# Optimization experiments

Hardware: AMD Instinct MI355X
Metric: run time of the kernel (lower is better)

Reference implementation:

```python
import jax, jax.numpy as jnp
import numpy as np

SHAPES = [(96, 96), (48, 48), (24, 24), (12, 12)]
B, C, NH, NP, NL, LYR, DFF = 4, 256, 8, 3, 4, 3, 1024
HD = C // NH
N = sum(h * w for h, w in SHAPES)


def setup_inputs():
    ks = iter(jax.random.split(jax.random.key(0), 64))
    p = lambda shape, s=0.02: jax.random.normal(next(ks), shape, jnp.float32) * s
    d = {}
    for i, (h, w) in enumerate(SHAPES):
        d[f'src{i}'] = jax.random.normal(next(ks), (B, C, h, w), jnp.float32)
        d[f'mask{i}'] = jnp.zeros((B, h, w), jnp.bool_)
        d[f'pos{i}'] = jax.random.normal(next(ks), (B, C, h, w), jnp.float32) * 0.02
    d['level_embed'] = p((NL, C), 1.0)  # torch init: normal_(std=1)
    d['W_off'] = p((LYR, C, NH * NL * NP * 2), 0.05); d['b_off'] = p((LYR, NH * NL * NP * 2), 0.05)
    d['W_attw'] = p((LYR, C, NH * NL * NP)); d['b_attw'] = jnp.zeros((LYR, NH * NL * NP))
    d['W_val'] = p((LYR, C, C)); d['b_val'] = jnp.zeros((LYR, C))
    d['W_out'] = p((LYR, C, C)); d['b_out'] = jnp.zeros((LYR, C))
    d['ln1_g'] = jnp.ones((LYR, C)); d['ln1_b'] = jnp.zeros((LYR, C))
    d['W_ff1'] = p((LYR, C, DFF)); d['b_ff1'] = jnp.zeros((LYR, DFF))
    d['W_ff2'] = p((LYR, DFF, C)); d['b_ff2'] = jnp.zeros((LYR, C))
    d['ln2_g'] = jnp.ones((LYR, C)); d['ln2_b'] = jnp.zeros((LYR, C))
    d['lnf_g'] = jnp.ones((C,)); d['lnf_b'] = jnp.zeros((C,))
    return d


def _layer_norm(x, g, b, eps=1e-5):
    m = jnp.mean(x, -1, keepdims=True)
    v = jnp.var(x, -1, keepdims=True)
    return (x - m) * jax.lax.rsqrt(v + eps) * g + b


def _ref_points():
    # centers of each cell per level, normalized to [0,1]; xy order -> [N,4] boxes with wh=0.1
    pts = []
    for h, w in SHAPES:
        ys = (jnp.arange(h, dtype=jnp.float32) + 0.5) / h
        xs = (jnp.arange(w, dtype=jnp.float32) + 0.5) / w
        yy, xx = jnp.meshgrid(ys, xs, indexing='ij')
        pts.append(jnp.stack([xx.ravel(), yy.ravel()], -1))
    r = jnp.concatenate(pts, 0)
    return jnp.concatenate([r, jnp.full_like(r, 0.1)], -1)


def _bilinear(value, H, W, loc):
    # value [B,H*W,NH,HD]; loc [B,Q,NH,NP,2] normalized; align_corners=False, zero padding
    x = loc[..., 0] * W - 0.5
    y = loc[..., 1] * H - 0.5
    x0f = jnp.floor(x); y0f = jnp.floor(y)
    wx = x - x0f; wy = y - y0f
    x0 = x0f.astype(jnp.int32); y0 = y0f.astype(jnp.int32)
    vt = jnp.transpose(value, (0, 2, 1, 3))  # [B,NH,HW,HD]
    Bq, Q = loc.shape[0], loc.shape[1]

    def g(yi, xi):
        valid = ((xi >= 0) & (xi < W) & (yi >= 0) & (yi < H)).astype(value.dtype)
        idx = jnp.clip(yi, 0, H - 1) * W + jnp.clip(xi, 0, W - 1)  # [B,Q,NH,NP]
        it = jnp.transpose(idx, (0, 2, 1, 3)).reshape(Bq, NH, Q * NP, 1)
        it = jnp.broadcast_to(it, (Bq, NH, Q * NP, HD))
        v = jnp.take_along_axis(vt, it, axis=2).reshape(Bq, NH, Q, NP, HD)
        v = jnp.transpose(v, (0, 2, 1, 3, 4))  # [B,Q,NH,NP,HD]
        return v * valid[..., None]

    return (g(y0, x0) * ((1 - wy) * (1 - wx))[..., None]
            + g(y0, x0 + 1) * ((1 - wy) * wx)[..., None]
            + g(y0 + 1, x0) * (wy * (1 - wx))[..., None]
            + g(y0 + 1, x0 + 1) * (wy * wx)[..., None])


def _msda(q, x, mask, ref, l, W_off, b_off, W_attw, b_attw, W_val, b_val, W_out, b_out):
    Bq, Nq, _ = q.shape
    value = x @ W_val[l] + b_val[l]
    value = jnp.where(mask[..., None], 0.0, value).reshape(Bq, Nq, NH, HD)
    off = (q @ W_off[l] + b_off[l]).reshape(Bq, Nq, NH, NL, NP, 2)
    aw = jax.nn.softmax((q @ W_attw[l] + b_attw[l]).reshape(Bq, Nq, NH, NL * NP), -1)
    aw = aw.reshape(Bq, Nq, NH, NL, NP)
    ref_xy = ref[None, :, None, None, None, :2]
    ref_wh = ref[None, :, None, None, None, 2:]
    loc = ref_xy + off / NP * ref_wh * 0.5  # [B,N,NH,NL,NP,2]
    out = jnp.zeros((Bq, Nq, NH, HD), x.dtype)
    s0 = 0
    for li, (h, w) in enumerate(SHAPES):
        samp = _bilinear(value[:, s0:s0 + h * w], h, w, loc[:, :, :, li])
        out = out + jnp.einsum('bqhpd,bqhp->bqhd', samp, aw[:, :, :, li])
        s0 += h * w
    return out.reshape(Bq, Nq, C) @ W_out[l] + b_out[l]


def _forward(srcs, masks, poss, level_embed, W_off, b_off, W_attw, b_attw, W_val, b_val,
             W_out, b_out, ln1_g, ln1_b, W_ff1, b_ff1, W_ff2, b_ff2, ln2_g, ln2_b, lnf_g, lnf_b):
    x = jnp.concatenate([s.reshape(B, C, -1).transpose(0, 2, 1) for s in srcs], 1)  # [B,N,C]
    mf = jnp.concatenate([m.reshape(B, -1) for m in masks], 1)                      # [B,N]
    pf = jnp.concatenate([p_.reshape(B, C, -1).transpose(0, 2, 1) + level_embed[i]
                          for i, p_ in enumerate(poss)], 1)
    ref = _ref_points()
    for l in range(LYR):
        q = x + pf
        x2 = _msda(q, x, mf, ref, l, W_off, b_off, W_attw, b_attw, W_val, b_val, W_out, b_out)
        x = _layer_norm(x + x2, ln1_g[l], ln1_b[l])
        h = jax.nn.gelu(x @ W_ff1[l] + b_ff1[l], approximate=False)
        x = _layer_norm(x + h @ W_ff2[l] + b_ff2[l], ln2_g[l], ln2_b[l])
    return _layer_norm(x, lnf_g, lnf_b)


def reference(src0, src1, src2, src3, mask0, mask1, mask2, mask3, pos0, pos1, pos2, pos3,
              level_embed, W_off, b_off, W_attw, b_attw, W_val, b_val, W_out, b_out,
              ln1_g, ln1_b, W_ff1, b_ff1, W_ff2, b_ff2, ln2_g, ln2_b, lnf_g, lnf_b):
    return _forward([src0, src1, src2, src3], [mask0, mask1, mask2, mask3],
                    [pos0, pos1, pos2, pos3], level_embed, W_off, b_off, W_attw, b_attw,
                    W_val, b_val, W_out, b_out, ln1_g, ln1_b, W_ff1, b_ff1, W_ff2, b_ff2,
                    ln2_g, ln2_b, lnf_g, lnf_b)
```

## Files before the change

### kernel.cpp

```cpp
#include <hip/hip_runtime.h>

#define B_   4
#define C_   256
#define NH_  8
#define HD_  32
#define NP_  3
#define NL_  4
#define LYR_ 3
#define DFF_ 1024
#define N_   12240
#define M_   (B_*N_)
#define MP_  49152
#define LT_  729088

typedef __attribute__((ext_vector_type(8))) short short8;
typedef __attribute__((ext_vector_type(4))) float f32x4;

__device__ __forceinline__ unsigned short f2bf(float f) {
    union { float f; unsigned u; } v; v.f = f;
    unsigned r = (v.u + 0x7fffu + ((v.u >> 16) & 1u)) >> 16;
    return (unsigned short)r;
}
__device__ __forceinline__ float bf2f(unsigned short h) {
    union { unsigned u; float f; } v; v.u = ((unsigned)h) << 16;
    return v.f;
}

__global__ __launch_bounds__(256) void k_concat_t(
    const float* __restrict__ s0, const float* __restrict__ s1,
    const float* __restrict__ s2, const float* __restrict__ s3,
    const float* __restrict__ p0, const float* __restrict__ p1,
    const float* __restrict__ p2, const float* __restrict__ p3,
    const float* __restrict__ lev,
    unsigned short* __restrict__ xh, unsigned short* __restrict__ xl,
    float* __restrict__ pf)
{
    const int z = blockIdx.z;
    const int b = z >> 2, li = z & 3;
    const int HWs[4]  = {9216, 2304, 576, 144};
    const int offs[4] = {0, 9216, 11520, 12096};
    const int HW = HWs[li];
    const int s0i = blockIdx.x * 32;
    if (s0i >= HW) return;
    const int ct = blockIdx.y * 32;
    const float* sp = (li == 0) ? s0 : (li == 1) ? s1 : (li == 2) ? s2 : s3;
    const float* pp = (li == 0) ? p0 : (li == 1) ? p1 : (li == 2) ? p2 : p3;

    __shared__ float tsx[32][33], tsp[32][33];
    const int tid = threadIdx.x;
    const int tc  = tid & 31;
    const int tr0 = tid >> 5;

    #pragma unroll
    for (int r = 0; r < 4; ++r) {
        int cl = tr0 + r * 8;
        int s  = s0i + tc;
        float vx = 0.f, vp = 0.f;
        if (s < HW) {
            size_t o = (size_t)(b * C_ + ct + cl) * HW + s;
            vx = sp[o]; vp = pp[o];
        }
        tsx[cl][tc] = vx; tsp[cl][tc] = vp;
    }
    __syncthreads();
    const float lv = lev[li * C_ + ct + tc];
    #pragma unroll
    for (int r = 0; r < 4; ++r) {
        int sl = tr0 + r * 8;
        int s  = s0i + sl;
        if (s < HW) {
            int row = b * N_ + offs[li] + s;
            size_t o = (size_t)row * C_ + ct + tc;
            float vx = tsx[tc][sl];
            unsigned short h = f2bf(vx);
            xh[o] = h;
            xl[o] = f2bf(vx - bf2f(h));
            pf[o] = tsp[tc][sl] + lv;
        }
    }
}

__global__ __launch_bounds__(256) void k_mask(
    float* __restrict__ v,
    const unsigned char* __restrict__ m0, const unsigned char* __restrict__ m1,
    const unsigned char* __restrict__ m2, const unsigned char* __restrict__ m3)
{
    int row = blockIdx.x;
    int n = row % N_, b = row / N_;
    int s, HW; const unsigned char* mp;
    if (n < 9216)       { s = n;         HW = 9216; mp = m0; }
    else if (n < 11520) { s = n - 9216;  HW = 2304; mp = m1; }
    else if (n < 12096) { s = n - 11520; HW = 576;  mp = m2; }
    else                { s = n - 12096; HW = 144;  mp = m3; }
    if (mp[b * HW + s])
        v[(size_t)row * C_ + threadIdx.x] = 0.f;
}

__global__ __launch_bounds__(256) void k_split(
    const float* __restrict__ W, unsigned short* __restrict__ Th,
    unsigned short* __restrict__ Tl, int K, int N)
{
    int per = K * N;
    int idx = blockIdx.x * 256 + threadIdx.x;
    if (idx >= LYR_ * per) return;
    int l = idx / per, r = idx - l * per;
    int k = r / N, n = r - k * N;
    float v = W[idx];
    unsigned short h = f2bf(v);
    unsigned short lo = f2bf(v - bf2f(h));
    size_t o = (size_t)l * LT_ + (size_t)n * K + k;
    Th[o] = h; Tl[o] = lo;
}

__device__ __forceinline__ int swz(int row, int bcol) {
    return row * 128 + (bcol ^ ((row & 7) << 4));
}

template <int MODE, int AKIND>
__global__ __launch_bounds__(256) void k_mgemm(
    const unsigned short* __restrict__ Ah, const unsigned short* __restrict__ Al,
    const float* __restrict__ A2f,
    const unsigned short* __restrict__ Bh, const unsigned short* __restrict__ Bl,
    const float* __restrict__ bias, const float* __restrict__ bias2, int bsplit,
    float* __restrict__ Cf, unsigned short* __restrict__ Ch,
    unsigned short* __restrict__ Cl, int Ndim, int Kdim)
{
    __shared__ __align__(16) unsigned short Ahs[128 * 64];
    __shared__ __align__(16) unsigned short Als[128 * 64];
    __shared__ __align__(16) unsigned short Bhs[128 * 64];
    __shared__ __align__(16) unsigned short Bls[128 * 64];

    const int tid = threadIdx.x;
    const int bm = blockIdx.y * 128;
    const int bn = blockIdx.x * 128;
    const int w  = tid >> 6, lane = tid & 63;
    const int wr = w >> 1, wc = w & 1;
    const int lm = lane & 15, lg = lane >> 4;

    const int srow = tid >> 1;
    const int sbc  = (tid & 1) * 64;

    f32x4 acc[4][4] = {};

    for (int k0 = 0; k0 < Kdim; k0 += 64) {
        {
            const unsigned short* ahp = Ah + (size_t)(bm + srow) * Kdim + k0 + (sbc >> 1);
            const unsigned short* alp = Al + (size_t)(bm + srow) * Kdim + k0 + (sbc >> 1);
            if (AKIND == 0) {
                #pragma unroll
                for (int q = 0; q < 4; ++q) {
                    short8 hv = *(const short8*)(ahp + q * 8);
                    short8 lv = *(const short8*)(alp + q * 8);
                    int o = swz(srow, sbc + q * 16) >> 1;
                    *(short8*)&Ahs[o] = hv;
                    *(short8*)&Als[o] = lv;
                }
            } else {
                const float* a2p = A2f + (size_t)(bm + srow) * Kdim + k0 + (sbc >> 1);
                #pragma unroll
                for (int q = 0; q < 4; ++q) {
                    short8 h8 = *(const short8*)(ahp + q * 8);
                    short8 l8 = *(const short8*)(alp + q * 8);
                    float4 u0 = *(const float4*)(a2p + q * 8);
                    float4 u1 = *(const float4*)(a2p + q * 8 + 4);
                    float f[8] = {u0.x, u0.y, u0.z, u0.w, u1.x, u1.y, u1.z, u1.w};
                    short8 hv, lv;
                    #pragma unroll
                    for (int j = 0; j < 8; ++j) {
                        float v = f[j] + bf2f((unsigned short)h8[j]) + bf2f((unsigned short)l8[j]);
                        unsigned short h = f2bf(v);
                        hv[j] = (short)h;
                        lv[j] = (short)f2bf(v - bf2f(h));
                    }
                    int o = swz(srow, sbc + q * 16) >> 1;
                    *(short8*)&Ahs[o] = hv;
                    *(short8*)&Als[o] = lv;
                }
            }
        }
        {
            int ng = bn + srow;
            bool ok = ng < Ndim;
            const unsigned short* bhp = Bh + (size_t)ng * Kdim + k0 + (sbc >> 1);
            const unsigned short* blp = Bl + (size_t)ng * Kdim + k0 + (sbc >> 1);
            #pragma unroll
            for (int q = 0; q < 4; ++q) {
                short8 hv = {}, lv = {};
                if (ok) {
                    hv = *(const short8*)(bhp + q * 8);
                    lv = *(const short8*)(blp + q * 8);
                }
                int o = swz(srow, sbc + q * 16) >> 1;
                *(short8*)&Bhs[o] = hv;
                *(short8*)&Bls[o] = lv;
            }
        }
        __syncthreads();
        #pragma unroll
        for (int ks = 0; ks < 2; ++ks) {
            const int cb = ks * 64 + lg * 16;
            short8 ah[4], al[4], bh[4], bl[4];
            #pragma unroll
            for (int i = 0; i < 4; ++i) {
                int o = swz(wr * 64 + i * 16 + lm, cb) >> 1;
                ah[i] = *(const short8*)&Ahs[o];
                al[i] = *(const short8*)&Als[o];
            }
            #pragma unroll
            for (int j = 0; j < 4; ++j) {
                int o = swz(wc * 64 + j * 16 + lm, cb) >> 1;
                bh[j] = *(const short8*)&Bhs[o];
                bl[j] = *(const short8*)&Bls[o];
            }
            #pragma unroll
            for (int i = 0; i < 4; ++i)
                #pragma unroll
                for (int j = 0; j < 4; ++j) {
                    acc[i][j] = __builtin_amdgcn_mfma_f32_16x16x32_bf16(al[i], bh[j], acc[i][j], 0, 0, 0);
                    acc[i][j] = __builtin_amdgcn_mfma_f32_16x16x32_bf16(ah[i], bl[j], acc[i][j], 0, 0, 0);
                    acc[i][j] = __builtin_amdgcn_mfma_f32_16x16x32_bf16(ah[i], bh[j], acc[i][j], 0, 0, 0);
                }
        }
        __syncthreads();
    }

    #pragma unroll
    for (int j = 0; j < 4; ++j) {
        int col = bn + wc * 64 + j * 16 + lm;
        if (col < Ndim) {
            float bb = (col < bsplit) ? bias[col] : bias2[col - bsplit];
            #pragma unroll
            for (int i = 0; i < 4; ++i) {
                #pragma unroll
                for (int p = 0; p < 4; ++p) {
                    int row = bm + wr * 64 + i * 16 + lg * 4 + p;
                    float v = acc[i][j][p] + bb;
                    if (MODE == 1) {
                        v = 0.5f * v * (1.f + erff(v * 0.70710678118654752f));
                        unsigned short h = f2bf(v);
                        Ch[(size_t)row * Ndim + col] = h;
                        Cl[(size_t)row * Ndim + col] = f2bf(v - bf2f(h));
                    } else {
                        Cf[(size_t)row * Ndim + col] = v;
                    }
                }
            }
        }
    }
}

__global__ __launch_bounds__(256) void k_sample(
    const float* __restrict__ value, const float* __restrict__ comb,
    unsigned short* __restrict__ msh, unsigned short* __restrict__ msl)
{
    int t = blockIdx.x * 256 + threadIdx.x;
    int gid = t >> 3;
    int q4  = t & 7;
    int h  = gid & 7;
    int bn = gid >> 3;
    int n  = bn % N_;
    int b  = bn / N_;

    int sr, Wr;
    if (n < 9216)       { sr = n;         Wr = 96; }
    else if (n < 11520) { sr = n - 9216;  Wr = 48; }
    else if (n < 12096) { sr = n - 11520; Wr = 24; }
    else                { sr = n - 12096; Wr = 12; }
    int iy = sr / Wr, ix = sr % Wr;
    float refx = (ix + 0.5f) / Wr;
    float refy = (iy + 0.5f) / Wr;

    const float* rowp = comb + (size_t)bn * 288;
    const float* offp = rowp + h * 24;
    const float* lgp  = rowp + 192 + h * 12;

    float lv[12];
    float mx = lgp[0];
    lv[0] = mx;
    #pragma unroll
    for (int i = 1; i < 12; ++i) { lv[i] = lgp[i]; mx = fmaxf(mx, lv[i]); }
    float ssum = 0.f;
    #pragma unroll
    for (int i = 0; i < 12; ++i) { lv[i] = __expf(lv[i] - mx); ssum += lv[i]; }
    float sinv = 1.f / ssum;

    const float* vbase = value + ((size_t)b * N_) * C_ + h * HD_ + q4 * 4;

    float4 acc = make_float4(0.f, 0.f, 0.f, 0.f);
    int s0 = 0;
    #pragma unroll
    for (int li = 0; li < 4; ++li) {
        const int Wl = 96 >> li;
        #pragma unroll
        for (int p = 0; p < NP_; ++p) {
            float ox = offp[(li * NP_ + p) * 2 + 0];
            float oy = offp[(li * NP_ + p) * 2 + 1];
            float xf = (refx + ox * (1.f / 60.f)) * Wl - 0.5f;
            float yf = (refy + oy * (1.f / 60.f)) * Wl - 0.5f;
            float x0f = floorf(xf), y0f = floorf(yf);
            float wx = xf - x0f, wy = yf - y0f;
            int x0 = (int)x0f, y0 = (int)y0f;
            float a = lv[li * NP_ + p] * sinv;
            #pragma unroll
            for (int dy = 0; dy < 2; ++dy) {
                #pragma unroll
                for (int dx = 0; dx < 2; ++dx) {
                    int yi = y0 + dy, xi = x0 + dx;
                    if (xi >= 0 && xi < Wl && yi >= 0 && yi < Wl) {
                        float wgt = a * (dy ? wy : 1.f - wy) * (dx ? wx : 1.f - wx);
                        float4 v = *(const float4*)(vbase + (size_t)(s0 + yi * Wl + xi) * C_);
                        acc.x += wgt * v.x; acc.y += wgt * v.y;
                        acc.z += wgt * v.z; acc.w += wgt * v.w;
                    }
                }
            }
        }
        s0 += Wl * Wl;
    }
    size_t ob = (size_t)gid * HD_ + q4 * 4;
    float a4[4] = {acc.x, acc.y, acc.z, acc.w};
    ushort4 hv, lv4;
    unsigned short* hp = (unsigned short*)&hv;
    unsigned short* lp = (unsigned short*)&lv4;
    #pragma unroll
    for (int j = 0; j < 4; ++j) {
        unsigned short hh = f2bf(a4[j]);
        hp[j] = hh;
        lp[j] = f2bf(a4[j] - bf2f(hh));
    }
    *(ushort4*)&msh[ob] = hv;
    *(ushort4*)&msl[ob] = lv4;
}

template <bool FINAL>
__global__ __launch_bounds__(256) void k_add_ln(
    unsigned short* __restrict__ xh, unsigned short* __restrict__ xl,
    const float* __restrict__ r,
    const float* __restrict__ g, const float* __restrict__ bta,
    float* __restrict__ outf)
{
    int row = blockIdx.x;
    int c = threadIdx.x;
    size_t o = (size_t)row * C_ + c;
    float v = bf2f(xh[o]) + bf2f(xl[o]) + (r ? r[o] : 0.f);
    float s1 = v, s2 = v * v;
    #pragma unroll
    for (int ofs = 32; ofs > 0; ofs >>= 1) {
        s1 += __shfl_down(s1, ofs);
        s2 += __shfl_down(s2, ofs);
    }
    __shared__ float r1[4], r2[4];
    int wid = threadIdx.x >> 6, lane = threadIdx.x & 63;
    if (lane == 0) { r1[wid] = s1; r2[wid] = s2; }
    __syncthreads();
    float m   = (r1[0] + r1[1] + r1[2] + r1[3]) * (1.f / C_);
    float var = (r2[0] + r2[1] + r2[2] + r2[3]) * (1.f / C_) - m * m;
    float inv = rsqrtf(var + 1e-5f);
    float y = (v - m) * inv * g[c] + bta[c];
    if (FINAL) {
        outf[o] = y;
    } else {
        unsigned short h = f2bf(y);
        xh[o] = h;
        xl[o] = f2bf(y - bf2f(h));
    }
}

extern "C" void kernel_launch(void* const* d_in, const int* in_sizes, int n_in,
                              void* d_out, int out_size, void* d_ws, size_t ws_size,
                              hipStream_t stream)
{
    const float* src0 = (const float*)d_in[0];
    const unsigned char* mask0 = (const unsigned char*)d_in[1];
    const float* pos0 = (const float*)d_in[2];
    const float* src1 = (const float*)d_in[3];
    const unsigned char* mask1 = (const unsigned char*)d_in[4];
    const float* pos1 = (const float*)d_in[5];
    const float* src2 = (const float*)d_in[6];
    const unsigned char* mask2 = (const unsigned char*)d_in[7];
    const float* pos2 = (const float*)d_in[8];
    const float* src3 = (const float*)d_in[9];
    const unsigned char* mask3 = (const unsigned char*)d_in[10];
    const float* pos3 = (const float*)d_in[11];
    const float* lev    = (const float*)d_in[12];
    const float* W_off  = (const float*)d_in[13];
    const float* b_off  = (const float*)d_in[14];
    const float* W_attw = (const float*)d_in[15];
    const float* b_attw = (const float*)d_in[16];
    const float* W_val  = (const float*)d_in[17];
    const float* b_val  = (const float*)d_in[18];
    const float* W_out  = (const float*)d_in[19];
    const float* b_out  = (const float*)d_in[20];
    const float* ln1_g  = (const float*)d_in[21];
    const float* ln1_b  = (const float*)d_in[22];
    const float* W_ff1  = (const float*)d_in[23];
    const float* b_ff1  = (const float*)d_in[24];
    const float* W_ff2  = (const float*)d_in[25];
    const float* b_ff2  = (const float*)d_in[26];
    const float* ln2_g  = (const float*)d_in[27];
    const float* ln2_b  = (const float*)d_in[28];
    const float* lnf_g  = (const float*)d_in[29];
    const float* lnf_b  = (const float*)d_in[30];

    float* ws = (float*)d_ws;
    auto at = [&](size_t u) { return ws + u * (size_t)MP_; };
    unsigned short* xh  = (unsigned short*)at(0);
    unsigned short* xl  = (unsigned short*)at(128);
    float* pf   = at(256);
    float* val  = at(512);
    unsigned short* msh = (unsigned short*)at(768);
    unsigned short* msl = (unsigned short*)at(896);
    float* comb = at(1024);
    float* tmp  = at(1024);
    unsigned short* hbh = (unsigned short*)at(512);
    unsigned short* hbl = hbh + (size_t)16384 * DFF_;

    unsigned short* Wh = (unsigned short*)(ws + (size_t)1312 * MP_);
    unsigned short* Wl = Wh + (size_t)LYR_ * LT_;
    const size_t OF_VAL = 0, OF_CMB = 65536, OF_ATT = 114688,
                 OF_OUT = 139264, OF_F1 = 204800, OF_F2 = 466944;

    const dim3 T(256);
    const int BIG = 1 << 30;

    k_split<<<(LYR_*65536 + 255)/256, T, 0, stream>>>(W_val,  Wh + OF_VAL, Wl + OF_VAL, 256, 256);
    k_split<<<(LYR_*49152 + 255)/256, T, 0, stream>>>(W_off,  Wh + OF_CMB, Wl + OF_CMB, 256, 192);
    k_split<<<(LYR_*24576 + 255)/256, T, 0, stream>>>(W_attw, Wh + OF_ATT, Wl + OF_ATT, 256, 96);
    k_split<<<(LYR_*65536 + 255)/256, T, 0, stream>>>(W_out,  Wh + OF_OUT, Wl + OF_OUT, 256, 256);
    k_split<<<(LYR_*262144 + 255)/256, T, 0, stream>>>(W_ff1, Wh + OF_F1,  Wl + OF_F1,  256, 1024);
    k_split<<<(LYR_*262144 + 255)/256, T, 0, stream>>>(W_ff2, Wh + OF_F2,  Wl + OF_F2,  1024, 256);

    k_concat_t<<<dim3(288, 8, 16), T, 0, stream>>>(
        src0, src1, src2, src3, pos0, pos1, pos2, pos3, lev, xh, xl, pf);

    for (int l = 0; l < LYR_; ++l) {
        const size_t lw = (size_t)l * LT_;

        k_mgemm<0, 0><<<dim3(2, MP_/128), T, 0, stream>>>(
            xh, xl, nullptr, Wh + lw + OF_VAL, Wl + lw + OF_VAL,
            b_val + l*C_, b_val + l*C_, BIG, val, nullptr, nullptr, 256, 256);
        k_mask<<<M_, T, 0, stream>>>(val, mask0, mask1, mask2, mask3);

        k_mgemm<0, 1><<<dim3(3, MP_/128), T, 0, stream>>>(
            xh, xl, pf, Wh + lw + OF_CMB, Wl + lw + OF_CMB,
            b_off + l*192, b_attw + l*96, 192, comb, nullptr, nullptr, 288, 256);

        k_sample<<<(M_*NH_*8)/256, T, 0, stream>>>(val, comb, msh, msl);

        k_mgemm<0, 0><<<dim3(2, MP_/128), T, 0, stream>>>(
            msh, msl, nullptr, Wh + lw + OF_OUT, Wl + lw + OF_OUT,
            b_out + l*C_, b_out + l*C_, BIG, tmp, nullptr, nullptr, 256, 256);

        k_add_ln<false><<<M_, T, 0, stream>>>(xh, xl, tmp, ln1_g + l*C_, ln1_b + l*C_, nullptr);

        for (int ch = 0; ch < 3; ++ch) {
            const size_t row0 = (size_t)ch * 16384;
            k_mgemm<1, 0><<<dim3(8, 128), T, 0, stream>>>(
                xh + row0*C_, xl + row0*C_, nullptr, Wh + lw + OF_F1, Wl + lw + OF_F1,
                b_ff1 + l*DFF_, b_ff1 + l*DFF_, BIG, nullptr, hbh, hbl, 1024, 256);
            k_mgemm<0, 0><<<dim3(2, 128), T, 0, stream>>>(
                hbh, hbl, nullptr, Wh + lw + OF_F2, Wl + lw + OF_F2,
                b_ff2 + l*C_, b_ff2 + l*C_, BIG, tmp + row0*C_, nullptr, nullptr, 256, 1024);
        }

        k_add_ln<false><<<M_, T, 0, stream>>>(xh, xl, tmp, ln2_g + l*C_, ln2_b + l*C_, nullptr);
    }

    k_add_ln<true><<<M_, T, 0, stream>>>(xh, xl, nullptr, lnf_g, lnf_b, (float*)d_out);
}
```

Before: 2.402 ms.

## Load GEMM tiles directly to LDS and remap sampler blocks across XCDs

```diff
diff --git a/kernel.cpp b/kernel.cpp
--- a/kernel.cpp
+++ b/kernel.cpp
@@ -26,6 +26,12 @@
     return v.f;
 }
 
+__device__ __forceinline__ void gload16(const void* g, void* lds) {
+    __builtin_amdgcn_global_load_lds(
+        (const __attribute__((address_space(1))) void*)g,
+        (__attribute__((address_space(3))) void*)lds, 16, 0, 0);
+}
+
 __global__ __launch_bounds__(256) void k_concat_t(
     const float* __restrict__ s0, const float* __restrict__ s1,
     const float* __restrict__ s2, const float* __restrict__ s3,
@@ -137,62 +143,61 @@
     const int wr = w >> 1, wc = w & 1;
     const int lm = lane & 15, lg = lane >> 4;
 
+    int grow[4], gsrc[4];
+    #pragma unroll
+    for (int q = 0; q < 4; ++q) {
+        int o = w * 4096 + q * 1024 + lane * 16;
+        int r = o >> 7;
+        grow[q] = r;
+        gsrc[q] = ((o & 127) ^ ((r & 7) << 4)) >> 1;
+    }
+
     const int srow = tid >> 1;
     const int sbc  = (tid & 1) * 64;
 
     f32x4 acc[4][4] = {};
 
     for (int k0 = 0; k0 < Kdim; k0 += 64) {
-        {
+        if (AKIND == 0) {
+            #pragma unroll
+            for (int q = 0; q < 4; ++q) {
+                size_t go = (size_t)(bm + grow[q]) * Kdim + k0 + gsrc[q];
+                char* lb = (char*)Ahs + w * 4096 + q * 1024;
+                gload16(Ah + go, lb);
+                gload16(Al + go, (char*)Als + w * 4096 + q * 1024);
+            }
+        } else {
             const unsigned short* ahp = Ah + (size_t)(bm + srow) * Kdim + k0 + (sbc >> 1);
             const unsigned short* alp = Al + (size_t)(bm + srow) * Kdim + k0 + (sbc >> 1);
-            if (AKIND == 0) {
+            const float* a2p = A2f + (size_t)(bm + srow) * Kdim + k0 + (sbc >> 1);
+            #pragma unroll
+            for (int q = 0; q < 4; ++q) {
+                short8 h8 = *(const short8*)(ahp + q * 8);
+                short8 l8 = *(const short8*)(alp + q * 8);
+                float4 u0 = *(const float4*)(a2p + q * 8);
+                float4 u1 = *(const float4*)(a2p + q * 8 + 4);
+                float f[8] = {u0.x, u0.y, u0.z, u0.w, u1.x, u1.y, u1.z, u1.w};
+                short8 hv, lv;
                 #pragma unroll
-                for (int q = 0; q < 4; ++q) {
-                    short8 hv = *(const short8*)(ahp + q * 8);
-                    short8 lv = *(const short8*)(alp + q * 8);
-                    int o = swz(srow, sbc + q * 16) >> 1;
-                    *(short8*)&Ahs[o] = hv;
-                    *(short8*)&Als[o] = lv;
-                }
-            } else {
-                const float* a2p = A2f + (size_t)(bm + srow) * Kdim + k0 + (sbc >> 1);
-                #pragma unroll
-                for (int q = 0; q < 4; ++q) {
-                    short8 h8 = *(const short8*)(ahp + q * 8);
-                    short8 l8 = *(const short8*)(alp + q * 8);
-                    float4 u0 = *(const float4*)(a2p + q * 8);
-                    float4 u1 = *(const float4*)(a2p + q * 8 + 4);
-                    float f[8] = {u0.x, u0.y, u0.z, u0.w, u1.x, u1.y, u1.z, u1.w};
-                    short8 hv, lv;
-                    #pragma unroll
-                    for (int j = 0; j < 8; ++j) {
-                        float v = f[j] + bf2f((unsigned short)h8[j]) + bf2f((unsigned short)l8[j]);
-                        unsigned short h = f2bf(v);
-                        hv[j] = (short)h;
-                        lv[j] = (short)f2bf(v - bf2f(h));
-                    }
-                    int o = swz(srow, sbc + q * 16) >> 1;
-                    *(short8*)&Ahs[o] = hv;
-                    *(short8*)&Als[o] = lv;
-                }
-            }
-        }
-        {
-            int ng = bn + srow;
-            bool ok = ng < Ndim;
-            const unsigned short* bhp = Bh + (size_t)ng * Kdim + k0 + (sbc >> 1);
-            const unsigned short* blp = Bl + (size_t)ng * Kdim + k0 + (sbc >> 1);
-            #pragma unroll
-            for (int q = 0; q < 4; ++q) {
-                short8 hv = {}, lv = {};
-                if (ok) {
-                    hv = *(const short8*)(bhp + q * 8);
-                    lv = *(const short8*)(blp + q * 8);
+                for (int j = 0; j < 8; ++j) {
+                    float v = f[j] + bf2f((unsigned short)h8[j]) + bf2f((unsigned short)l8[j]);
+                    unsigned short h = f2bf(v);
+                    hv[j] = (short)h;
+                    lv[j] = (short)f2bf(v - bf2f(h));
                 }
                 int o = swz(srow, sbc + q * 16) >> 1;
-                *(short8*)&Bhs[o] = hv;
-                *(short8*)&Bls[o] = lv;
+                *(short8*)&Ahs[o] = hv;
+                *(short8*)&Als[o] = lv;
+            }
+        }
+        {
+            #pragma unroll
+            for (int q = 0; q < 4; ++q) {
+                int nr = bn + grow[q];
+                if (nr >= Ndim) nr = Ndim - 1;
+                size_t go = (size_t)nr * Kdim + k0 + gsrc[q];
+                gload16(Bh + go, (char*)Bhs + w * 4096 + q * 1024);
+                gload16(Bl + go, (char*)Bls + w * 4096 + q * 1024);
             }
         }
         __syncthreads();
@@ -253,7 +258,11 @@
     const float* __restrict__ value, const float* __restrict__ comb,
     unsigned short* __restrict__ msh, unsigned short* __restrict__ msl)
 {
-    int t = blockIdx.x * 256 + threadIdx.x;
+    const int nwg = (M_ * NH_ * 8) / 256;
+    const int cpx = nwg >> 3;
+    int bid = blockIdx.x;
+    int sb  = (bid & 7) * cpx + (bid >> 3);
+    int t   = sb * 256 + threadIdx.x;
     int gid = t >> 3;
     int q4  = t & 7;
     int h  = gid & 7;
```

Measured after the change: 2.260 ms. -5.9%, faster.
